# Performance work log

Hardware: AMD Instinct MI355X
Metric: run time of the kernel (lower is better)

## Reference

```python
import jax, jax.numpy as jnp
import numpy as np

# dims (see shape_source)
B, N, P, H, M, E, HOPS = 512, 102, 12, 256, 4, 3, 2
C_CLIP = 10.0   # logit clipping constant params['C']
T = 1.0         # temperature params['T']
NEG = -1e9


def setup_inputs() -> dict:
    key = jax.random.key(0)
    ks = jax.random.split(key, 18)
    s = 0.08  # uniform init range as in _initialize_weights, use scaled normals
    inp = {
        "node_features": jax.random.normal(ks[0], (B, N, P), jnp.float32),
        "adjacency": jax.random.uniform(ks[1], (B, E, N, N), jnp.float32),  # per-edge-cat weighted adjacency
        "mask": jax.random.randint(ks[2], (B, N), 0, 2).astype(jnp.int32),  # 1 = already scheduled / forbidden
        # encoder params
        "W_emb": jax.random.normal(ks[3], (P, H), jnp.float32) * s,
        "W_rel": jax.random.normal(ks[4], (HOPS, E, H, H), jnp.float32) * s / np.sqrt(H),
        "W_self": jax.random.normal(ks[5], (HOPS, H, H), jnp.float32) * s / np.sqrt(H),
        # multi-head glimpse params (Vec / W_q / W_ref per head)
        "Vec": jax.random.normal(ks[6], (M, H, H), jnp.float32) * s,
        "W_q": jax.random.normal(ks[7], (M, 3 * H, H), jnp.float32) * s,
        "W_ref": jax.random.normal(ks[8], (M, H, H), jnp.float32) * s,
        "W_mh": jax.random.normal(ks[9], (M * H, H), jnp.float32) * s,  # multi_head_embedding
        # final pointer params
        "Vec2": jax.random.normal(ks[10], (H,), jnp.float32) * s,
        "W_q2": jax.random.normal(ks[11], (H, H), jnp.float32) * s,
        "W_ref2": jax.random.normal(ks[12], (H, H), jnp.float32) * s,
        # learned decoder seed vectors
        "dec_input": jax.random.normal(ks[13], (H,), jnp.float32) * s,
        "v_1": jax.random.normal(ks[14], (H,), jnp.float32) * s,
    }
    return inp


def reference(node_features, adjacency, mask, W_emb, W_rel, W_self, Vec, W_q,
              W_ref, W_mh, Vec2, W_q2, W_ref2, dec_input, v_1):
    # ---- encoder: linear embedding + HOPS of relational (per-edge-category) message passing ----
    h = jnp.einsum('bnp,ph->bnh', node_features, W_emb)            # [B,N,H]
    for hop in range(HOPS):
        msg = jnp.einsum('benm,bmh->benh', adjacency, h)           # gather neighbors per edge cat
        h = jax.nn.relu(jnp.einsum('benh,ehk->bnk', msg, W_rel[hop])
                        + jnp.einsum('bnh,hk->bnk', h, W_self[hop]))
    enc = h                                                         # [B,N,H]

    # ---- decoder query: cat(graph readout, learned dec_input, learned v_1) -> 3H ----
    enc_mean = enc.mean(axis=1)                                     # [B,H]
    q_cat = jnp.concatenate([enc_mean,
                             jnp.broadcast_to(dec_input, (B, H)),
                             jnp.broadcast_to(v_1, (B, H))], axis=-1)  # [B,3H]

    # ---- multi-head additive (Bahdanau) glimpse: per-head Vec/W_q/W_ref tanh scoring ----
    q = jnp.einsum('bf,mfh->bmh', q_cat, W_q)                       # [B,M,H]
    r = jnp.einsum('bnh,mhk->bmnk', enc, W_ref)                     # [B,M,N,H]
    u = jnp.einsum('bmnh,mhk->bmnk', jnp.tanh(q[:, :, None, :] + r), Vec)
    scores = u.sum(axis=-1)                                         # [B,M,N]
    scores = jnp.where(mask[:, None, :] > 0, NEG, scores)
    a = jax.nn.softmax(scores, axis=-1)
    ctx = jnp.einsum('bmn,bnh->bmh', a, enc).reshape(B, M * H)
    query2 = ctx @ W_mh                                             # [B,H]

    # ---- final pointer head (Vec2 / W_q2 / W_ref2) ----
    u2 = jnp.einsum('h,bnh->bn', Vec2,
                    jnp.tanh((query2 @ W_q2)[:, None, :] + jnp.einsum('bnh,hk->bnk', enc, W_ref2)))
    u2 = C_CLIP * jnp.tanh(u2)                                      # logit clipping
    u2 = jnp.where(mask > 0, NEG, u2)
    log_p = jax.nn.log_softmax(u2 / T, axis=-1)                     # [B,N]
    return log_p
```

## Files before the change

### kernel.cpp

```cpp
#include <hip/hip_runtime.h>
#include <hip/hip_bf16.h>

#define B 512
#define N 102
#define Pdim 12
#define H 256
#define M 4
#define E 3
#define NEG (-1e9f)
#define RT 52224
#define NN 10404

typedef __hip_bfloat16 bf16;
typedef __attribute__((ext_vector_type(8))) short short8;
typedef __attribute__((ext_vector_type(4))) float f32x4;
typedef __attribute__((ext_vector_type(16))) float f32x16;

__device__ __forceinline__ float b2f(bf16 v) { return __bfloat162float(v); }
__device__ __forceinline__ bf16 f2b(float v) { return __float2bfloat16(v); }
__device__ __forceinline__ short f2bs(float v) {
    bf16 t = __float2bfloat16(v);
    return *reinterpret_cast<short*>(&t);
}
__device__ __forceinline__ float fast_tanh(float x) {
    float e = __expf(2.f * x);
    return 1.f - 2.f * __builtin_amdgcn_rcpf(e + 1.f);
}

__global__ __launch_bounds__(256) void wt_prep(const float* __restrict__ Wrel,
                                               const float* __restrict__ Wself,
                                               const float* __restrict__ Wref,
                                               const float* __restrict__ Wref2,
                                               const float* __restrict__ Wmh,
                                               const float* __restrict__ Wq2,
                                               const float* __restrict__ W_q,
                                               const float* __restrict__ Vec,
                                               const float* __restrict__ W_emb,
                                               const float* __restrict__ dec,
                                               const float* __restrict__ v1,
                                               const float* __restrict__ adj,
                                               short* __restrict__ wfrag,
                                               short* __restrict__ wrefT,
                                               short* __restrict__ wref2T,
                                               short* __restrict__ wmh_bf,
                                               short* __restrict__ wq2_bf,
                                               short* __restrict__ wq_bf,
                                               short* __restrict__ wembf,
                                               short* __restrict__ adjp,
                                               float* __restrict__ qconst,
                                               float* __restrict__ vsum) {
    int bid = blockIdx.x;
    int tid = threadIdx.x;
    __shared__ short tl[1024 * 17];
    if (bid >= 3652) {
        int be = bid - 3652;
        const float* src = adj + (size_t)be * NN;
        short* dst = adjp + (size_t)be * (112 * 128);
        for (int i = tid; i < 112 * 128; i += 256) {
            int n = i >> 7, m = i & 127;
            short v = 0;
            if (n < N && m < N) v = f2bs(src[n * N + m]);
            dst[i] = v;
        }
        return;
    }
    if (bid < 32) {
        int hop = bid >> 4, ct = bid & 15;
        for (int i = tid; i < 16384; i += 256) {
            int k = i >> 4, c0 = i & 15;
            int c = ct * 16 + c0;
            float v;
            if (k < 768) v = Wrel[(((size_t)hop * E + (k >> 8)) * H + (k & 255)) * H + c];
            else         v = Wself[((size_t)hop * H + (k - 768)) * H + c];
            tl[k * 17 + c0] = f2bs(v);
        }
        __syncthreads();
        short8* outp = (short8*)wfrag + (size_t)(hop * 16 + ct) * 2048;
        for (int i = tid; i < 2048; i += 256) {
            int ks = i >> 6, lq = i & 63;
            int c0 = lq & 15, kb = (lq >> 4) * 8;
            short8 v;
#pragma unroll
            for (int j = 0; j < 8; ++j) v[j] = tl[(ks * 32 + kb + j) * 17 + c0];
            outp[i] = v;
        }
        return;
    }
    if (bid >= 3648) {
        int m = bid - 3648, hh = tid;
        __shared__ float dls[H], vls[H];
        dls[hh] = dec[hh];
        vls[hh] = v1[hh];
        __syncthreads();
        const float* Wm = W_q + (size_t)m * (3 * H) * H;
        float s = 0.f;
        for (int f = 0; f < H; ++f)
            s += dls[f] * Wm[(H + f) * H + hh] + vls[f] * Wm[(2 * H + f) * H + hh];
        qconst[m * H + hh] = s;
        float vs = 0.f;
        const float* Vr = Vec + ((size_t)m * H + hh) * H;
        for (int k = 0; k < H; ++k) vs += Vr[k];
        vsum[m * H + hh] = vs;
        return;
    }
    int idx = 524288 + (bid - 32) * 256 + tid;
    if (idx < 786432) {
        int r = idx - 524288;
        int row = r >> 8, k = r & 255;
        int m = row >> 8, c = row & 255;
        wrefT[r] = f2bs(Wref[((size_t)m * H + k) * H + c]);
    } else if (idx < 851968) {
        int r = idx - 786432;
        int c = r >> 8, k = r & 255;
        wref2T[r] = f2bs(Wref2[k * H + c]);
    } else if (idx < 1114112) {
        int r = idx - 851968;
        wmh_bf[r] = f2bs(Wmh[r]);
    } else if (idx < 1179648) {
        int r = idx - 1114112;
        wq2_bf[r] = f2bs(Wq2[r]);
    } else if (idx < 1441792) {
        int r = idx - 1179648;
        int m = r >> 16, fh = r & 65535;
        wq_bf[r] = f2bs(W_q[(size_t)m * 768 * 256 + fh]);
    } else if (idx < 1449984) {
        int r = idx - 1441792;
        int ct = r >> 9, lq = (r >> 3) & 63, j = r & 7;
        int c = ct * 16 + (lq & 15), k = (lq >> 4) * 8 + j;
        wembf[r] = (k < Pdim) ? f2bs(W_emb[k * H + c]) : (short)0;
    }
}

#define HP 264
#define YP2 136
#define ASP 136
__global__ __launch_bounds__(512, 2) void enc_fused(const float* __restrict__ nf,
                                                    const short* __restrict__ wembf,
                                                    const short* __restrict__ adjp,
                                                    const short* __restrict__ wfragp,
                                                    bf16* __restrict__ enc_out,
                                                    float* __restrict__ mean_out) {
    int b = blockIdx.x;
    int tid = threadIdx.x;
    int w = tid >> 6;
    int l = tid & 63;
    int cg = l & 15;
    int rg = l >> 4;
    int ct0 = 2 * w, ct1 = ct0 + 1;

    __shared__ short hS[112 * HP];
    __shared__ short YtS[256 * YP2];
    __shared__ short AsS[112 * ASP];

    const short8 z8 = {0, 0, 0, 0, 0, 0, 0, 0};
    for (int i = tid; i < 10 * 32; i += 512) {
        int n = 102 + (i >> 5), g = i & 31;
        *(short8*)(&hS[n * HP + g * 8]) = z8;
    }
    {
        int c = tid >> 1, g = 14 + (tid & 1);
        *(short8*)(&YtS[c * YP2 + g * 8]) = z8;
    }

    {
        const short8* we8 = (const short8*)wembf;
        short8 bfe0 = we8[ct0 * 64 + l];
        short8 bfe1 = we8[ct1 * 64 + l];
#pragma unroll
        for (int nt = 0; nt < 7; ++nt) {
            int row = nt * 16 + cg;
            short8 afr = z8;
            if (row < 102 && rg < 2) {
                const float* src = nf + ((size_t)b * N + row) * Pdim + rg * 8;
                f32x4 v0 = *(const f32x4*)src;
                afr[0] = f2bs(v0[0]); afr[1] = f2bs(v0[1]);
                afr[2] = f2bs(v0[2]); afr[3] = f2bs(v0[3]);
                if (rg == 0) {
                    f32x4 v1 = *(const f32x4*)(src + 4);
                    afr[4] = f2bs(v1[0]); afr[5] = f2bs(v1[1]);
                    afr[6] = f2bs(v1[2]); afr[7] = f2bs(v1[3]);
                }
            }
            f32x4 d0 = (f32x4){0.f, 0.f, 0.f, 0.f}, d1 = d0;
            d0 = __builtin_amdgcn_mfma_f32_16x16x32_bf16(afr, bfe0, d0, 0, 0, 0);
            d1 = __builtin_amdgcn_mfma_f32_16x16x32_bf16(afr, bfe1, d1, 0, 0, 0);
#pragma unroll
            for (int r = 0; r < 4; ++r) {
                int n = nt * 16 + rg * 4 + r;
                hS[n * HP + ct0 * 16 + cg] = f2bs(d0[r]);
                hS[n * HP + ct1 * 16 + cg] = f2bs(d1[r]);
            }
        }
    }
    __syncthreads();

    for (int hop = 0; hop < 2; ++hop) {
        const short8* wf8 = ((const short8*)wfragp) + (size_t)hop * 32768;
        f32x4 hacc0[7], hacc1[7];
#pragma unroll
        for (int j = 0; j < 7; ++j) {
            hacc0[j] = (f32x4){0.f, 0.f, 0.f, 0.f};
            hacc1[j] = hacc0[j];
        }

        for (int e = 0; e < E; ++e) {
            const short8* Ap = (const short8*)adjp + (size_t)(b * E + e) * 1792;
            for (int i = tid; i < 1792; i += 512) {
                int n = i >> 4, g = i & 15;
                *(short8*)(&AsS[n * ASP + g * 8]) = Ap[i];
            }
            if (e == 0) {
#pragma unroll
                for (int ks = 0; ks < 8; ++ks) {
                    short8 wfs0 = wf8[(ct0 * 32 + 24 + ks) * 64 + l];
                    short8 wfs1 = wf8[(ct1 * 32 + 24 + ks) * 64 + l];
#pragma unroll
                    for (int nt = 0; nt < 7; ++nt) {
                        short8 hf = *(const short8*)(&hS[(nt * 16 + cg) * HP + ks * 32 + rg * 8]);
                        hacc0[nt] = __builtin_amdgcn_mfma_f32_16x16x32_bf16(hf, wfs0, hacc0[nt], 0, 0, 0);
                        hacc1[nt] = __builtin_amdgcn_mfma_f32_16x16x32_bf16(hf, wfs1, hacc1[nt], 0, 0, 0);
                    }
                }
            }
            f32x4 g0[7], g1[7];
#pragma unroll
            for (int j = 0; j < 7; ++j) {
                g0[j] = (f32x4){0.f, 0.f, 0.f, 0.f};
                g1[j] = g0[j];
            }
#pragma unroll
            for (int ks = 0; ks < 8; ++ks) {
                short8 wfa0 = wf8[(ct0 * 32 + e * 8 + ks) * 64 + l];
                short8 wfa1 = wf8[(ct1 * 32 + e * 8 + ks) * 64 + l];
#pragma unroll
                for (int mt = 0; mt < 7; ++mt) {
                    short8 hf = *(const short8*)(&hS[(mt * 16 + cg) * HP + ks * 32 + rg * 8]);
                    g0[mt] = __builtin_amdgcn_mfma_f32_16x16x32_bf16(wfa0, hf, g0[mt], 0, 0, 0);
                    g1[mt] = __builtin_amdgcn_mfma_f32_16x16x32_bf16(wfa1, hf, g1[mt], 0, 0, 0);
                }
            }
#pragma unroll
            for (int mt = 0; mt < 7; ++mt)
#pragma unroll
                for (int r = 0; r < 4; ++r) {
                    int c0 = ct0 * 16 + rg * 4 + r;
                    int c1 = ct1 * 16 + rg * 4 + r;
                    YtS[c0 * YP2 + mt * 16 + cg] = f2bs(g0[mt][r]);
                    YtS[c1 * YP2 + mt * 16 + cg] = f2bs(g1[mt][r]);
                }
            __syncthreads();
#pragma unroll
            for (int ks = 0; ks < 4; ++ks) {
                short8 yf0 = *(const short8*)(&YtS[(ct0 * 16 + cg) * YP2 + (ks * 4 + rg) * 8]);
                short8 yf1 = *(const short8*)(&YtS[(ct1 * 16 + cg) * YP2 + (ks * 4 + rg) * 8]);
#pragma unroll
                for (int nt = 0; nt < 7; ++nt) {
                    short8 af = *(const short8*)(&AsS[(nt * 16 + cg) * ASP + ks * 32 + rg * 8]);
                    hacc0[nt] = __builtin_amdgcn_mfma_f32_16x16x32_bf16(af, yf0, hacc0[nt], 0, 0, 0);
                    hacc1[nt] = __builtin_amdgcn_mfma_f32_16x16x32_bf16(af, yf1, hacc1[nt], 0, 0, 0);
                }
            }
            __syncthreads();
        }
#pragma unroll
        for (int nt = 0; nt < 7; ++nt)
#pragma unroll
            for (int r = 0; r < 4; ++r) {
                int n = nt * 16 + rg * 4 + r;
                float v0 = hacc0[nt][r], v1 = hacc1[nt][r];
                hS[n * HP + ct0 * 16 + cg] = f2bs(v0 > 0.f ? v0 : 0.f);
                hS[n * HP + ct1 * 16 + cg] = f2bs(v1 > 0.f ? v1 : 0.f);
            }
        __syncthreads();
    }

    short* ho = (short*)enc_out;
    for (int i = tid; i < 102 * 32; i += 512) {
        int n = i >> 5, g = i & 31;
        *(short8*)(ho + ((size_t)b * N + n) * H + g * 8) = *(const short8*)(&hS[n * HP + g * 8]);
    }
    {
        float* partf = (float*)AsS;
        int c = tid & 255, qq = tid >> 8;
        float s = 0.f;
        for (int n = qq; n < N; n += 2) s += b2f(*(const bf16*)&hS[n * HP + c]);
        partf[qq * 256 + c] = s;
        __syncthreads();
        if (tid < 256)
            mean_out[(size_t)b * H + tid] = (partf[tid] + partf[256 + tid]) * (1.f / (float)N);
    }
}

__global__ __launch_bounds__(256, 2) void head2_mfma(const bf16* __restrict__ X,
                                                     const short* __restrict__ WT,
                                                     const float* __restrict__ qb, int qbs,
                                                     const float* __restrict__ vsb,
                                                     float* __restrict__ outp, int obs,
                                                     int mcnt) {
    int rt = blockIdx.x;
    int r0 = rt * 128;
    int tid = threadIdx.x;
    int w = tid >> 6, l = tid & 63;
    int lr = l & 31;
    int lh = l >> 5;
    __shared__ short Xs[128 * 256];
    __shared__ float qls[12 * 256];
    __shared__ float part[4][128];

    const short* Xp = (const short*)X;
#pragma unroll
    for (int i = 0; i < 16; ++i) {
        int id = tid + i * 256;
        int r = id >> 5, g = id & 31;
        short8 v = *(const short8*)(Xp + (size_t)(r0 + r) * H + g * 8);
        *(short8*)((char*)Xs + r * 512 + ((g ^ (r & 7)) * 16)) = v;
    }
    int b_base = r0 / N;
    for (int i = tid; i < 3 * mcnt * 256; i += 256) {
        int boff = i / (mcnt * 256);
        int rem = i - boff * (mcnt * 256);
        int m = rem >> 8, c = rem & 255;
        int bb = b_base + boff;
        if (bb > B - 1) bb = B - 1;
        qls[(boff * mcnt + m) * 256 + c] = qb[(size_t)bb * qbs + m * H + c];
    }
    __syncthreads();

    int swz = lr & 7;
    for (int m = 0; m < mcnt; ++m) {
        const short8* w8 = (const short8*)(WT + (size_t)m * H * H);
        int cbase = w * 64;
        short8 afr0[16], afr1[16];
#pragma unroll
        for (int ks = 0; ks < 16; ++ks) {
            afr0[ks] = w8[(size_t)(cbase + lr) * 32 + ks * 2 + lh];
            afr1[ks] = w8[(size_t)(cbase + 32 + lr) * 32 + ks * 2 + lh];
        }
        float vsl[32];
#pragma unroll
        for (int j = 0; j < 16; ++j) {
            int cl = (j & 3) + 8 * (j >> 2) + 4 * lh;
            vsl[j]      = vsb[m * H + w * 64 + cl];
            vsl[16 + j] = vsb[m * H + w * 64 + 32 + cl];
        }
        for (int t = 0; t < 4; ++t) {
            f32x16 acc0, acc1;
#pragma unroll
            for (int j = 0; j < 16; ++j) { acc0[j] = 0.f; acc1[j] = 0.f; }
            const char* xbase = (const char*)Xs + (t * 32 + lr) * 512;
#pragma unroll
            for (int ks = 0; ks < 16; ++ks) {
                short8 bx = *(const short8*)(xbase + (((2 * ks + lh) ^ swz) * 16));
                acc0 = __builtin_amdgcn_mfma_f32_32x32x16_bf16(afr0[ks], bx, acc0, 0, 0, 0);
                acc1 = __builtin_amdgcn_mfma_f32_32x32x16_bf16(afr1[ks], bx, acc1, 0, 0, 0);
            }
            int r = r0 + t * 32 + lr;
            int b = r / N;
            int boff = b - b_base;
            const float* qrow = &qls[(boff * mcnt + m) * 256];
            float s = 0.f;
#pragma unroll
            for (int j = 0; j < 16; ++j) {
                int cl = (j & 3) + 8 * (j >> 2) + 4 * lh;
                float x0 = qrow[w * 64 + cl] + acc0[j];
                s += fast_tanh(x0) * vsl[j];
                float x1 = qrow[w * 64 + 32 + cl] + acc1[j];
                s += fast_tanh(x1) * vsl[16 + j];
            }
            s += __shfl_xor(s, 32, 64);
            if (l < 32) part[w][t * 32 + lr] = s;
        }
        __syncthreads();
        if (tid < 128) {
            int r = r0 + tid;
            int b = r / N, n = r - b * N;
            outp[(size_t)b * obs + m * N + n] = part[0][tid] + part[1][tid] + part[2][tid] + part[3][tid];
        }
        __syncthreads();
    }
}

__global__ __launch_bounds__(256) void q_k(const float* __restrict__ enc_mean,
                                           const short* __restrict__ wq_bf,
                                           const float* __restrict__ qconst,
                                           float* __restrict__ qbuf) {
    int bid = blockIdx.x;
    int b = bid >> 2, m = bid & 3;
    int hh = threadIdx.x;
    __shared__ float em[H];
    em[hh] = enc_mean[(size_t)b * H + hh];
    __syncthreads();
    const bf16* Wm = (const bf16*)(wq_bf + (size_t)m * 65536);
    float s = qconst[m * H + hh];
    for (int f = 0; f < H; ++f) s += em[f] * b2f(Wm[f * H + hh]);
    qbuf[((size_t)b * M + m) * H + hh] = s;
}

__global__ __launch_bounds__(256) void softmax_ctx_k(const float* __restrict__ scores,
                                                     const int* __restrict__ mask,
                                                     const bf16* __restrict__ enc,
                                                     float* __restrict__ ctx) {
    int b = blockIdx.x;
    int tid = threadIdx.x;
    int w = tid >> 6;
    int l = tid & 63;
    __shared__ short hEnc[102 * 264];
    __shared__ float a[M][112];
    __shared__ float red[M];

    const short* ep = (const short*)enc;
    for (int i = tid; i < 102 * 32; i += 256) {
        int n = i >> 5, g = i & 31;
        *(short8*)(&hEnc[n * 264 + g * 8]) = *(const short8*)(ep + ((size_t)b * N + n) * H + g * 8);
    }
    for (int i = tid; i < M * 112; i += 256) {
        int m = i / 112, n = i % 112;
        float s = NEG;
        if (n < N) s = (mask[(size_t)b * N + n] > 0) ? NEG : scores[((size_t)b * M + m) * N + n];
        a[m][n] = s;
    }
    __syncthreads();
    {
        float v = a[w][l];
        float v2 = (l + 64 < 112) ? a[w][l + 64] : NEG;
        v = fmaxf(v, v2);
        v = fmaxf(v, __shfl_xor(v, 32, 64));
        v = fmaxf(v, __shfl_xor(v, 16, 64));
        v = fmaxf(v, __shfl_xor(v, 8, 64));
        v = fmaxf(v, __shfl_xor(v, 4, 64));
        v = fmaxf(v, __shfl_xor(v, 2, 64));
        v = fmaxf(v, __shfl_xor(v, 1, 64));
        float mx = __shfl(v, 0, 64);
        float e0 = __expf(a[w][l] - mx);
        float e1 = (l + 64 < 112) ? __expf(a[w][l + 64] - mx) : 0.f;
        a[w][l] = e0;
        if (l + 64 < 112) a[w][l + 64] = e1;
        float sv = e0 + e1;
        sv += __shfl_xor(sv, 32, 64);
        sv += __shfl_xor(sv, 16, 64);
        sv += __shfl_xor(sv, 8, 64);
        sv += __shfl_xor(sv, 4, 64);
        sv += __shfl_xor(sv, 2, 64);
        sv += __shfl_xor(sv, 1, 64);
        if (l == 0) red[w] = __builtin_amdgcn_rcpf(sv);
    }
    __syncthreads();
    float c0 = 0.f, c1 = 0.f, c2 = 0.f, c3 = 0.f;
    for (int n = 0; n < N; ++n) {
        float e = b2f(*(const bf16*)&hEnc[n * 264 + tid]);
        c0 += a[0][n] * e;
        c1 += a[1][n] * e;
        c2 += a[2][n] * e;
        c3 += a[3][n] * e;
    }
    ctx[((size_t)b * M + 0) * H + tid] = c0 * red[0];
    ctx[((size_t)b * M + 1) * H + tid] = c1 * red[1];
    ctx[((size_t)b * M + 2) * H + tid] = c2 * red[2];
    ctx[((size_t)b * M + 3) * H + tid] = c3 * red[3];
}

__global__ __launch_bounds__(256) void query2_k(const float* __restrict__ ctx,
                                                const short* __restrict__ wmh,
                                                const short* __restrict__ wq2,
                                                float* __restrict__ q2) {
    int b = blockIdx.x;
    int tid = threadIdx.x;
    __shared__ float cx[M * H];
    __shared__ float qy[H];
    for (int idx = tid; idx < M * H; idx += 256) cx[idx] = ctx[(size_t)b * M * H + idx];
    __syncthreads();
    const bf16* wm = (const bf16*)wmh;
    float acc = 0.f;
    for (int j = 0; j < M * H; ++j) acc += cx[j] * b2f(wm[(size_t)j * H + tid]);
    qy[tid] = acc;
    __syncthreads();
    const bf16* w2 = (const bf16*)wq2;
    float acc2 = 0.f;
    for (int k = 0; k < H; ++k) acc2 += qy[k] * b2f(w2[(size_t)k * H + tid]);
    q2[(size_t)b * H + tid] = acc2;
}

__global__ __launch_bounds__(128) void final_out_k(const float* __restrict__ u2,
                                                   const int* __restrict__ mask,
                                                   float* __restrict__ out) {
    int b = blockIdx.x;
    int tid = threadIdx.x;
    __shared__ float a[128];
    __shared__ float red[2];
    float u = NEG;
    if (tid < N) {
        u = 10.f * fast_tanh(u2[(size_t)b * N + tid]);
        if (mask[(size_t)b * N + tid] > 0) u = NEG;
    }
    a[tid] = u;
    __syncthreads();
    if (tid < 64) {
        float v = fmaxf(a[tid], a[tid + 64]);
        v = fmaxf(v, __shfl_xor(v, 32, 64));
        v = fmaxf(v, __shfl_xor(v, 16, 64));
        v = fmaxf(v, __shfl_xor(v, 8, 64));
        v = fmaxf(v, __shfl_xor(v, 4, 64));
        v = fmaxf(v, __shfl_xor(v, 2, 64));
        v = fmaxf(v, __shfl_xor(v, 1, 64));
        if (tid == 0) red[0] = v;
    }
    __syncthreads();
    float mx = red[0];
    float ev = (tid < N) ? __expf(u - mx) : 0.f;
    a[tid] = ev;
    __syncthreads();
    if (tid < 64) {
        float v = a[tid] + a[tid + 64];
        v += __shfl_xor(v, 32, 64);
        v += __shfl_xor(v, 16, 64);
        v += __shfl_xor(v, 8, 64);
        v += __shfl_xor(v, 4, 64);
        v += __shfl_xor(v, 2, 64);
        v += __shfl_xor(v, 1, 64);
        if (tid == 0) red[1] = logf(v);
    }
    __syncthreads();
    if (tid < N) out[(size_t)b * N + tid] = (u - mx) - red[1];
}

extern "C" void kernel_launch(void* const* d_in, const int* in_sizes, int n_in,
                              void* d_out, int out_size, void* d_ws, size_t ws_size,
                              hipStream_t stream) {
    const float* nf     = (const float*)d_in[0];
    const float* adj    = (const float*)d_in[1];
    const int*   mask   = (const int*)d_in[2];
    const float* W_emb  = (const float*)d_in[3];
    const float* W_rel  = (const float*)d_in[4];
    const float* W_self = (const float*)d_in[5];
    const float* Vec    = (const float*)d_in[6];
    const float* W_q    = (const float*)d_in[7];
    const float* W_ref  = (const float*)d_in[8];
    const float* W_mh   = (const float*)d_in[9];
    const float* Vec2   = (const float*)d_in[10];
    const float* W_q2   = (const float*)d_in[11];
    const float* W_ref2 = (const float*)d_in[12];
    const float* dec    = (const float*)d_in[13];
    const float* v_1    = (const float*)d_in[14];
    float* out = (float*)d_out;

    char* p = (char*)d_ws;
    size_t off = 0;
    auto alloc = [&](size_t bytes) -> char* {
        char* q = p + off;
        off += (bytes + 255) & ~(size_t)255;
        return q;
    };
    bf16* hA      = (bf16*)alloc((size_t)RT * H * sizeof(bf16));
    short* adjp   = (short*)alloc((size_t)B * E * 112 * 128 * sizeof(short));
    short* wfrag  = (short*)alloc(524288 * sizeof(short));
    short* wrefT  = (short*)alloc(262144 * sizeof(short));
    short* wref2T = (short*)alloc(65536 * sizeof(short));
    short* wmh_bf = (short*)alloc(262144 * sizeof(short));
    short* wq2_bf = (short*)alloc(65536 * sizeof(short));
    short* wq_bf  = (short*)alloc(262144 * sizeof(short));
    short* wembf  = (short*)alloc(8192 * sizeof(short));
    float* enc_mean = (float*)alloc((size_t)B * H * sizeof(float));
    float* qconst   = (float*)alloc((size_t)M * H * sizeof(float));
    float* vsumb    = (float*)alloc((size_t)M * H * sizeof(float));
    float* qbuf     = (float*)alloc((size_t)B * M * H * sizeof(float));
    float* scoresb  = (float*)alloc((size_t)B * M * N * sizeof(float));
    float* ctxb     = (float*)alloc((size_t)B * M * H * sizeof(float));
    float* q2b      = (float*)alloc((size_t)B * H * sizeof(float));
    float* u2b      = (float*)alloc((size_t)B * N * sizeof(float));

    wt_prep<<<5188, 256, 0, stream>>>(W_rel, W_self, W_ref, W_ref2, W_mh, W_q2,
                                      W_q, Vec, W_emb, dec, v_1, adj,
                                      wfrag, wrefT, wref2T, wmh_bf, wq2_bf, wq_bf, wembf,
                                      adjp, qconst, vsumb);

    enc_fused<<<B, 512, 0, stream>>>(nf, wembf, adjp, wfrag, hA, enc_mean);

    const bf16* enc = hA;

    q_k<<<B * M, 256, 0, stream>>>(enc_mean, wq_bf, qconst, qbuf);
    head2_mfma<<<RT / 128, 256, 0, stream>>>(enc, wrefT, qbuf, M * H, vsumb, scoresb, M * N, M);
    softmax_ctx_k<<<B, 256, 0, stream>>>(scoresb, mask, enc, ctxb);
    query2_k<<<B, 256, 0, stream>>>(ctxb, wmh_bf, wq2_bf, q2b);
    head2_mfma<<<RT / 128, 256, 0, stream>>>(enc, wref2T, q2b, H, Vec2, u2b, N, 1);
    final_out_k<<<B, 128, 0, stream>>>(u2b, mask, out);
}
```

Measured before the change: 269.2 us.

## Retile encoder MFMA warps and batch query projections across 16 batch rows

Encoder warps now each own 4 column tiles across 3-4 row tiles instead of 2 column tiles across all 7 row tiles, which changes how fragments are reused from shared memory. The q and query2 projection kernels now process 16 batch elements per block, so weight matrices are read once per group rather than once per batch row. This cuts redundant global weight traffic. The cost is far fewer blocks (32 for query2), which may lower parallelism, and more registers per thread.

```diff
diff --git a/kernel.cpp b/kernel.cpp
--- a/kernel.cpp
+++ b/kernel.cpp
@@ -146,7 +146,11 @@
     int l = tid & 63;
     int cg = l & 15;
     int rg = l >> 4;
-    int ct0 = 2 * w, ct1 = ct0 + 1;
+    int q = w & 3;
+    int halfsel = w >> 2;
+    int ctb = 4 * q;
+    int nt0 = halfsel * 4;
+    int ntc = halfsel ? 3 : 4;
 
     __shared__ short hS[112 * HP];
     __shared__ short YtS[256 * YP2];
@@ -164,31 +168,36 @@
 
     {
         const short8* we8 = (const short8*)wembf;
-        short8 bfe0 = we8[ct0 * 64 + l];
-        short8 bfe1 = we8[ct1 * 64 + l];
-#pragma unroll
-        for (int nt = 0; nt < 7; ++nt) {
-            int row = nt * 16 + cg;
-            short8 afr = z8;
-            if (row < 102 && rg < 2) {
-                const float* src = nf + ((size_t)b * N + row) * Pdim + rg * 8;
-                f32x4 v0 = *(const f32x4*)src;
-                afr[0] = f2bs(v0[0]); afr[1] = f2bs(v0[1]);
-                afr[2] = f2bs(v0[2]); afr[3] = f2bs(v0[3]);
-                if (rg == 0) {
-                    f32x4 v1 = *(const f32x4*)(src + 4);
-                    afr[4] = f2bs(v1[0]); afr[5] = f2bs(v1[1]);
-                    afr[6] = f2bs(v1[2]); afr[7] = f2bs(v1[3]);
+        short8 bfe[4];
+#pragma unroll
+        for (int cj = 0; cj < 4; ++cj) bfe[cj] = we8[(ctb + cj) * 64 + l];
+#pragma unroll
+        for (int jt = 0; jt < 4; ++jt) {
+            if (jt < ntc) {
+                int nt = nt0 + jt;
+                int row = nt * 16 + cg;
+                short8 afr = z8;
+                if (row < 102 && rg < 2) {
+                    const float* src = nf + ((size_t)b * N + row) * Pdim + rg * 8;
+                    f32x4 v0 = *(const f32x4*)src;
+                    afr[0] = f2bs(v0[0]); afr[1] = f2bs(v0[1]);
+                    afr[2] = f2bs(v0[2]); afr[3] = f2bs(v0[3]);
+                    if (rg == 0) {
+                        f32x4 v1 = *(const f32x4*)(src + 4);
+                        afr[4] = f2bs(v1[0]); afr[5] = f2bs(v1[1]);
+                        afr[6] = f2bs(v1[2]); afr[7] = f2bs(v1[3]);
+                    }
                 }
-            }
-            f32x4 d0 = (f32x4){0.f, 0.f, 0.f, 0.f}, d1 = d0;
-            d0 = __builtin_amdgcn_mfma_f32_16x16x32_bf16(afr, bfe0, d0, 0, 0, 0);
-            d1 = __builtin_amdgcn_mfma_f32_16x16x32_bf16(afr, bfe1, d1, 0, 0, 0);
-#pragma unroll
-            for (int r = 0; r < 4; ++r) {
-                int n = nt * 16 + rg * 4 + r;
-                hS[n * HP + ct0 * 16 + cg] = f2bs(d0[r]);
-                hS[n * HP + ct1 * 16 + cg] = f2bs(d1[r]);
+#pragma unroll
+                for (int cj = 0; cj < 4; ++cj) {
+                    f32x4 d = (f32x4){0.f, 0.f, 0.f, 0.f};
+                    d = __builtin_amdgcn_mfma_f32_16x16x32_bf16(afr, bfe[cj], d, 0, 0, 0);
+#pragma unroll
+                    for (int r = 0; r < 4; ++r) {
+                        int n = nt * 16 + rg * 4 + r;
+                        hS[n * HP + (ctb + cj) * 16 + cg] = f2bs(d[r]);
+                    }
+                }
             }
         }
     }
@@ -196,12 +205,11 @@
 
     for (int hop = 0; hop < 2; ++hop) {
         const short8* wf8 = ((const short8*)wfragp) + (size_t)hop * 32768;
-        f32x4 hacc0[7], hacc1[7];
-#pragma unroll
-        for (int j = 0; j < 7; ++j) {
-            hacc0[j] = (f32x4){0.f, 0.f, 0.f, 0.f};
-            hacc1[j] = hacc0[j];
-        }
+        f32x4 hacc[4][4];
+#pragma unroll
+        for (int cj = 0; cj < 4; ++cj)
+#pragma unroll
+            for (int jt = 0; jt < 4; ++jt) hacc[cj][jt] = (f32x4){0.f, 0.f, 0.f, 0.f};
 
         for (int e = 0; e < E; ++e) {
             const short8* Ap = (const short8*)adjp + (size_t)(b * E + e) * 1792;
@@ -212,65 +220,93 @@
             if (e == 0) {
 #pragma unroll
                 for (int ks = 0; ks < 8; ++ks) {
-                    short8 wfs0 = wf8[(ct0 * 32 + 24 + ks) * 64 + l];
-                    short8 wfs1 = wf8[(ct1 * 32 + 24 + ks) * 64 + l];
-#pragma unroll
-                    for (int nt = 0; nt < 7; ++nt) {
-                        short8 hf = *(const short8*)(&hS[(nt * 16 + cg) * HP + ks * 32 + rg * 8]);
-                        hacc0[nt] = __builtin_amdgcn_mfma_f32_16x16x32_bf16(hf, wfs0, hacc0[nt], 0, 0, 0);
-                        hacc1[nt] = __builtin_amdgcn_mfma_f32_16x16x32_bf16(hf, wfs1, hacc1[nt], 0, 0, 0);
+                    short8 wfs[4];
+#pragma unroll
+                    for (int cj = 0; cj < 4; ++cj)
+                        wfs[cj] = wf8[((ctb + cj) * 32 + 24 + ks) * 64 + l];
+#pragma unroll
+                    for (int jt = 0; jt < 4; ++jt) {
+                        if (jt < ntc) {
+                            int nt = nt0 + jt;
+                            short8 hf = *(const short8*)(&hS[(nt * 16 + cg) * HP + ks * 32 + rg * 8]);
+#pragma unroll
+                            for (int cj = 0; cj < 4; ++cj)
+                                hacc[cj][jt] = __builtin_amdgcn_mfma_f32_16x16x32_bf16(hf, wfs[cj], hacc[cj][jt], 0, 0, 0);
+                        }
                     }
                 }
             }
-            f32x4 g0[7], g1[7];
-#pragma unroll
-            for (int j = 0; j < 7; ++j) {
-                g0[j] = (f32x4){0.f, 0.f, 0.f, 0.f};
-                g1[j] = g0[j];
-            }
-#pragma unroll
-            for (int ks = 0; ks < 8; ++ks) {
-                short8 wfa0 = wf8[(ct0 * 32 + e * 8 + ks) * 64 + l];
-                short8 wfa1 = wf8[(ct1 * 32 + e * 8 + ks) * 64 + l];
-#pragma unroll
-                for (int mt = 0; mt < 7; ++mt) {
-                    short8 hf = *(const short8*)(&hS[(mt * 16 + cg) * HP + ks * 32 + rg * 8]);
-                    g0[mt] = __builtin_amdgcn_mfma_f32_16x16x32_bf16(wfa0, hf, g0[mt], 0, 0, 0);
-                    g1[mt] = __builtin_amdgcn_mfma_f32_16x16x32_bf16(wfa1, hf, g1[mt], 0, 0, 0);
+            for (int ch = 0; ch < ntc; ch += 2) {
+                int cnt = (ntc - ch < 2) ? (ntc - ch) : 2;
+                f32x4 g[4][2];
+#pragma unroll
+                for (int cj = 0; cj < 4; ++cj) {
+                    g[cj][0] = (f32x4){0.f, 0.f, 0.f, 0.f};
+                    g[cj][1] = g[cj][0];
                 }
-            }
-#pragma unroll
-            for (int mt = 0; mt < 7; ++mt)
-#pragma unroll
-                for (int r = 0; r < 4; ++r) {
-                    int c0 = ct0 * 16 + rg * 4 + r;
-                    int c1 = ct1 * 16 + rg * 4 + r;
-                    YtS[c0 * YP2 + mt * 16 + cg] = f2bs(g0[mt][r]);
-                    YtS[c1 * YP2 + mt * 16 + cg] = f2bs(g1[mt][r]);
+#pragma unroll
+                for (int ks = 0; ks < 8; ++ks) {
+                    short8 wfa[4];
+#pragma unroll
+                    for (int cj = 0; cj < 4; ++cj)
+                        wfa[cj] = wf8[((ctb + cj) * 32 + e * 8 + ks) * 64 + l];
+#pragma unroll
+                    for (int jt = 0; jt < 2; ++jt) {
+                        if (jt < cnt) {
+                            int mt = nt0 + ch + jt;
+                            short8 hf = *(const short8*)(&hS[(mt * 16 + cg) * HP + ks * 32 + rg * 8]);
+#pragma unroll
+                            for (int cj = 0; cj < 4; ++cj)
+                                g[cj][jt] = __builtin_amdgcn_mfma_f32_16x16x32_bf16(wfa[cj], hf, g[cj][jt], 0, 0, 0);
+                        }
+                    }
                 }
+#pragma unroll
+                for (int jt = 0; jt < 2; ++jt) {
+                    if (jt < cnt) {
+                        int mt = nt0 + ch + jt;
+#pragma unroll
+                        for (int cj = 0; cj < 4; ++cj)
+#pragma unroll
+                            for (int r = 0; r < 4; ++r)
+                                YtS[((ctb + cj) * 16 + rg * 4 + r) * YP2 + mt * 16 + cg] = f2bs(g[cj][jt][r]);
+                    }
+                }
+            }
             __syncthreads();
 #pragma unroll
             for (int ks = 0; ks < 4; ++ks) {
-                short8 yf0 = *(const short8*)(&YtS[(ct0 * 16 + cg) * YP2 + (ks * 4 + rg) * 8]);
-                short8 yf1 = *(const short8*)(&YtS[(ct1 * 16 + cg) * YP2 + (ks * 4 + rg) * 8]);
-#pragma unroll
-                for (int nt = 0; nt < 7; ++nt) {
-                    short8 af = *(const short8*)(&AsS[(nt * 16 + cg) * ASP + ks * 32 + rg * 8]);
-                    hacc0[nt] = __builtin_amdgcn_mfma_f32_16x16x32_bf16(af, yf0, hacc0[nt], 0, 0, 0);
-                    hacc1[nt] = __builtin_amdgcn_mfma_f32_16x16x32_bf16(af, yf1, hacc1[nt], 0, 0, 0);
+                short8 yf[4];
+#pragma unroll
+                for (int cj = 0; cj < 4; ++cj)
+                    yf[cj] = *(const short8*)(&YtS[((ctb + cj) * 16 + cg) * YP2 + (ks * 4 + rg) * 8]);
+#pragma unroll
+                for (int jt = 0; jt < 4; ++jt) {
+                    if (jt < ntc) {
+                        int nt = nt0 + jt;
+                        short8 af = *(const short8*)(&AsS[(nt * 16 + cg) * ASP + ks * 32 + rg * 8]);
+#pragma unroll
+                        for (int cj = 0; cj < 4; ++cj)
+                            hacc[cj][jt] = __builtin_amdgcn_mfma_f32_16x16x32_bf16(af, yf[cj], hacc[cj][jt], 0, 0, 0);
+                    }
                 }
             }
             __syncthreads();
         }
 #pragma unroll
-        for (int nt = 0; nt < 7; ++nt)
-#pragma unroll
-            for (int r = 0; r < 4; ++r) {
-                int n = nt * 16 + rg * 4 + r;
-                float v0 = hacc0[nt][r], v1 = hacc1[nt][r];
-                hS[n * HP + ct0 * 16 + cg] = f2bs(v0 > 0.f ? v0 : 0.f);
-                hS[n * HP + ct1 * 16 + cg] = f2bs(v1 > 0.f ? v1 : 0.f);
-            }
+        for (int jt = 0; jt < 4; ++jt) {
+            if (jt < ntc) {
+                int nt = nt0 + jt;
+#pragma unroll
+                for (int cj = 0; cj < 4; ++cj)
+#pragma unroll
+                    for (int r = 0; r < 4; ++r) {
+                        int n = nt * 16 + rg * 4 + r;
+                        float v = hacc[cj][jt][r];
+                        hS[n * HP + (ctb + cj) * 16 + cg] = f2bs(v > 0.f ? v : 0.f);
+                    }
+            }
+        }
         __syncthreads();
     }
 
@@ -380,20 +416,30 @@
     }
 }
 
-__global__ __launch_bounds__(256) void q_k(const float* __restrict__ enc_mean,
-                                           const short* __restrict__ wq_bf,
-                                           const float* __restrict__ qconst,
-                                           float* __restrict__ qbuf) {
+__global__ __launch_bounds__(256) void q_k16(const float* __restrict__ enc_mean,
+                                             const short* __restrict__ wq_bf,
+                                             const float* __restrict__ qconst,
+                                             float* __restrict__ qbuf) {
     int bid = blockIdx.x;
-    int b = bid >> 2, m = bid & 3;
+    int bg = bid >> 2, m = bid & 3;
     int hh = threadIdx.x;
-    __shared__ float em[H];
-    em[hh] = enc_mean[(size_t)b * H + hh];
+    __shared__ float em[16][H];
+    for (int i = hh; i < 16 * H; i += 256)
+        em[i >> 8][i & 255] = enc_mean[((size_t)bg * 16 + (i >> 8)) * H + (i & 255)];
     __syncthreads();
     const bf16* Wm = (const bf16*)(wq_bf + (size_t)m * 65536);
-    float s = qconst[m * H + hh];
-    for (int f = 0; f < H; ++f) s += em[f] * b2f(Wm[f * H + hh]);
-    qbuf[((size_t)b * M + m) * H + hh] = s;
+    float qc = qconst[m * H + hh];
+    float acc[16];
+#pragma unroll
+    for (int bb = 0; bb < 16; ++bb) acc[bb] = qc;
+    for (int f = 0; f < H; ++f) {
+        float wv = b2f(Wm[f * H + hh]);
+#pragma unroll
+        for (int bb = 0; bb < 16; ++bb) acc[bb] += em[bb][f] * wv;
+    }
+#pragma unroll
+    for (int bb = 0; bb < 16; ++bb)
+        qbuf[(((size_t)bg * 16 + bb) * M + m) * H + hh] = acc[bb];
 }
 
 __global__ __launch_bounds__(256) void softmax_ctx_k(const float* __restrict__ scores,
@@ -459,25 +505,42 @@
     ctx[((size_t)b * M + 3) * H + tid] = c3 * red[3];
 }
 
-__global__ __launch_bounds__(256) void query2_k(const float* __restrict__ ctx,
-                                                const short* __restrict__ wmh,
-                                                const short* __restrict__ wq2,
-                                                float* __restrict__ q2) {
-    int b = blockIdx.x;
+__global__ __launch_bounds__(512) void query2_k16(const float* __restrict__ ctx,
+                                                  const short* __restrict__ wmh,
+                                                  const short* __restrict__ wq2,
+                                                  float* __restrict__ q2) {
+    int bg = blockIdx.x;
     int tid = threadIdx.x;
-    __shared__ float cx[M * H];
-    __shared__ float qy[H];
-    for (int idx = tid; idx < M * H; idx += 256) cx[idx] = ctx[(size_t)b * M * H + idx];
+    int col = tid & 255, bh = tid >> 8;
+    __shared__ float cx[16][M * H];
+    __shared__ float qy[16][H];
+    for (int i = tid; i < 16 * M * H; i += 512)
+        cx[i >> 10][i & 1023] = ctx[(size_t)bg * 16 * M * H + i];
     __syncthreads();
     const bf16* wm = (const bf16*)wmh;
-    float acc = 0.f;
-    for (int j = 0; j < M * H; ++j) acc += cx[j] * b2f(wm[(size_t)j * H + tid]);
-    qy[tid] = acc;
+    float acc[8];
+#pragma unroll
+    for (int u = 0; u < 8; ++u) acc[u] = 0.f;
+    for (int j = 0; j < M * H; ++j) {
+        float wv = b2f(wm[(size_t)j * H + col]);
+#pragma unroll
+        for (int u = 0; u < 8; ++u) acc[u] += cx[bh * 8 + u][j] * wv;
+    }
+#pragma unroll
+    for (int u = 0; u < 8; ++u) qy[bh * 8 + u][col] = acc[u];
     __syncthreads();
     const bf16* w2 = (const bf16*)wq2;
-    float acc2 = 0.f;
-    for (int k = 0; k < H; ++k) acc2 += qy[k] * b2f(w2[(size_t)k * H + tid]);
-    q2[(size_t)b * H + tid] = acc2;
+    float acc2[8];
+#pragma unroll
+    for (int u = 0; u < 8; ++u) acc2[u] = 0.f;
+    for (int k = 0; k < H; ++k) {
+        float wv2 = b2f(w2[(size_t)k * H + col]);
+#pragma unroll
+        for (int u = 0; u < 8; ++u) acc2[u] += qy[bh * 8 + u][k] * wv2;
+    }
+#pragma unroll
+    for (int u = 0; u < 8; ++u)
+        q2[((size_t)bg * 16 + bh * 8 + u) * H + col] = acc2[u];
 }
 
 __global__ __launch_bounds__(128) void final_out_k(const float* __restrict__ u2,
@@ -577,10 +640,10 @@
 
     const bf16* enc = hA;
 
-    q_k<<<B * M, 256, 0, stream>>>(enc_mean, wq_bf, qconst, qbuf);
+    q_k16<<<(B / 16) * M, 256, 0, stream>>>(enc_mean, wq_bf, qconst, qbuf);
     head2_mfma<<<RT / 128, 256, 0, stream>>>(enc, wrefT, qbuf, M * H, vsumb, scoresb, M * N, M);
     softmax_ctx_k<<<B, 256, 0, stream>>>(scoresb, mask, enc, ctxb);
-    query2_k<<<B, 256, 0, stream>>>(ctxb, wmh_bf, wq2_bf, q2b);
+    query2_k16<<<B / 16, 512, 0, stream>>>(ctxb, wmh_bf, wq2_bf, q2b);
     head2_mfma<<<RT / 128, 256, 0, stream>>>(enc, wref2T, q2b, H, Vec2, u2b, N, 1);
     final_out_k<<<B, 128, 0, stream>>>(u2b, mask, out);
 }
```

Result: slower. 456.4 us (+69.5%).
